# Kernel tuning notes

Hardware: AMD Instinct MI355X
Metric: run time of the kernel (lower is better)

## Reference

```python
import jax, jax.numpy as jnp
import numpy as np

EMB_DIM = 256
Q_DIM = 512
V_DIM = 512

def setup_inputs() -> dict:
    key = jax.random.key(0)
    ks = jax.random.split(key, 7)
    B, S = 8, 2048
    x = jax.random.normal(ks[0], (B, S, EMB_DIM), dtype=jnp.float32)
    s = 1.0 / np.sqrt(EMB_DIM)
    Wq = jax.random.normal(ks[1], (EMB_DIM, Q_DIM), dtype=jnp.float32) * s
    bq = jax.random.normal(ks[2], (Q_DIM,), dtype=jnp.float32) * 0.01
    Wk = jax.random.normal(ks[3], (EMB_DIM, Q_DIM), dtype=jnp.float32) * s
    bk = jax.random.normal(ks[4], (Q_DIM,), dtype=jnp.float32) * 0.01
    Wv = jax.random.normal(ks[5], (EMB_DIM, V_DIM), dtype=jnp.float32) * s
    bv = jax.random.normal(ks[6], (V_DIM,), dtype=jnp.float32) * 0.01
    return {"x": x, "Wq": Wq, "bq": bq, "Wk": Wk, "bk": bk, "Wv": Wv, "bv": bv}

def reference(x, Wq, bq, Wk, bk, Wv, bv):
    # q/k/v projections (torch Linear == x @ W + b with W stored [in, out] here)
    q = jax.nn.sigmoid(jnp.einsum('bse,eq->bsq', x, Wq) + bq)   # [B,S,Q]
    k = jnp.einsum('bse,eq->bsq', x, Wk) + bk                   # [B,S,Q]
    v = jnp.einsum('bse,ev->bsv', x, Wv) + bv                   # [B,S,V]
    scale = 1.0 / jnp.sqrt(jnp.float32(EMB_DIM))
    qk = jnp.einsum('bsq,btq->bst', q, k) * scale               # [B,S,S]
    qk = jax.nn.elu(qk)
    attn = jax.nn.softmax(qk, axis=-1)
    return jnp.einsum('bst,btv->bsv', attn, v)                  # [B,S,V]
```

## Files before the change

### kernel.cpp

```cpp
#include <hip/hip_runtime.h>
#include <hip/hip_bf16.h>
#include <math.h>

typedef unsigned short u16;
using short8 = __attribute__((ext_vector_type(8))) short;
using f32x4  = __attribute__((ext_vector_type(4))) float;

#define BM 128
#define BN 128
#define BK 32


__device__ __forceinline__ u16 f2bf(float f) {
  union { float f; unsigned u; } v; v.f = f;
  unsigned r = v.u + 0x7FFFu + ((v.u >> 16) & 1u);
  return (u16)(r >> 16);
}

__device__ __forceinline__ float fexp(float x) { return __expf(x); }

__device__ __forceinline__ void gld16(const void* g, void* l) {
  __builtin_amdgcn_global_load_lds(
      (const __attribute__((address_space(1))) void*)g,
      (__attribute__((address_space(3))) void*)l,
      16, 0, 0);
}


__device__ __forceinline__ void gemm_core(const u16* __restrict__ Ag,
                                          const u16* __restrict__ Bg,
                                          int K, u16* As, u16* Bs,
                                          f32x4 acc[4][4]) {
  const int tid = threadIdx.x;
  const int w = tid >> 6, l = tid & 63;
  const int wm = (w & 1) << 6, wn = (w >> 1) << 6;
  const int ln = l & 15, lq = l >> 4;
  const int sr0 = w * 16 + (l >> 2);
  const int sr1 = 64 + sr0;
  const int sk = (l & 3) * 8;

#pragma unroll
  for (int mt = 0; mt < 4; mt++)
#pragma unroll
    for (int nt = 0; nt < 4; nt++) acc[mt][nt] = (f32x4)0.0f;

  for (int k0 = 0; k0 < K; k0 += BK) {
    __syncthreads();
    gld16(Ag + (size_t)sr0 * K + k0 + sk, As + sr0 * BK + sk);
    gld16(Ag + (size_t)sr1 * K + k0 + sk, As + sr1 * BK + sk);
    gld16(Bg + (size_t)sr0 * K + k0 + sk, Bs + sr0 * BK + sk);
    gld16(Bg + (size_t)sr1 * K + k0 + sk, Bs + sr1 * BK + sk);
    __syncthreads();
    short8 af[4], bf[4];
#pragma unroll
    for (int mt = 0; mt < 4; mt++)
      af[mt] = *(const short8*)(As + (wm + mt * 16 + ln) * BK + lq * 8);
#pragma unroll
    for (int nt = 0; nt < 4; nt++)
      bf[nt] = *(const short8*)(Bs + (wn + nt * 16 + ln) * BK + lq * 8);
#pragma unroll
    for (int mt = 0; mt < 4; mt++)
#pragma unroll
      for (int nt = 0; nt < 4; nt++)
        acc[mt][nt] = __builtin_amdgcn_mfma_f32_16x16x32_bf16(
            af[mt], bf[nt], acc[mt][nt], 0, 0, 0);
  }
}


__global__ __launch_bounds__(256) void k_convx(const float* __restrict__ x,
                                               u16* __restrict__ xb, int n4) {
  int i = blockIdx.x * 256 + threadIdx.x;
  if (i < n4) {
    float4 v = ((const float4*)x)[i];
    ushort4 o;
    o.x = f2bf(v.x); o.y = f2bf(v.y); o.z = f2bf(v.z); o.w = f2bf(v.w);
    ((ushort4*)xb)[i] = o;
  }
}

__global__ __launch_bounds__(256) void k_convw(
    const float* __restrict__ Wq, const float* __restrict__ Wk,
    const float* __restrict__ Wv, const float* __restrict__ bq,
    const float* __restrict__ bk, const float* __restrict__ bv,
    u16* __restrict__ Wt, float* __restrict__ bcat) {
  int i = blockIdx.x * 256 + threadIdx.x;
  if (i < 1536 * 256) {
    int nn = i >> 8, e = i & 255;
    int sel = nn >> 9, c = nn & 511;
    const float* W = (sel == 0) ? Wq : (sel == 1) ? Wk : Wv;
    Wt[i] = f2bf(W[e * 512 + c]);
    if (e == 0) {
      const float* bb = (sel == 0) ? bq : (sel == 1) ? bk : bv;
      bcat[nn] = bb[c];
    }
  }
}


__global__ __launch_bounds__(256) void k_proj(
    const u16* __restrict__ xb, const u16* __restrict__ Wt,
    const float* __restrict__ bcat, u16* __restrict__ qb,
    u16* __restrict__ kb, u16* __restrict__ vb) {
  __shared__ __align__(16) u16 As[BM * BK];
  __shared__ __align__(16) u16 Bs[BN * BK];
  const int bm = blockIdx.y * BM, bn = blockIdx.x * BN;
  f32x4 acc[4][4];
  gemm_core(xb + (size_t)bm * 256, Wt + (size_t)bn * 256, 256, As, Bs, acc);

  const int tid = threadIdx.x, w = tid >> 6, l = tid & 63;
  const int wm = (w & 1) << 6, wn = (w >> 1) << 6;
  const int ln = l & 15, lq = l >> 4;
#pragma unroll
  for (int mt = 0; mt < 4; mt++)
#pragma unroll
    for (int r = 0; r < 4; r++) {
      int row = bm + wm + mt * 16 + lq * 4 + r;
#pragma unroll
      for (int nt = 0; nt < 4; nt++) {
        int col = bn + wn + nt * 16 + ln;
        float v = acc[mt][nt][r] + bcat[col];
        int sel = col >> 9, c2 = col & 511;
        float sg = __builtin_amdgcn_rcpf(1.0f + fexp(-v));
        float ov = (sel == 0) ? sg : v;
        u16* dst = (sel == 0) ? qb : (sel == 1) ? kb : vb;
        dst[(size_t)row * 512 + c2] = f2bf(ov);
      }
    }
}


__global__ __launch_bounds__(256) void k_transv(const u16* __restrict__ vb,
                                                u16* __restrict__ vtb) {
  const int b = blockIdx.z;
  const int t0 = blockIdx.y * 64, v0 = blockIdx.x * 64;
  __shared__ u16 tl[64][65];
  const u16* src = vb + (size_t)b * 2048 * 512;
  u16* dst = vtb + (size_t)b * 512 * 2048;
  for (int i = threadIdx.x; i < 4096; i += 256) {
    int r = i >> 6, c = i & 63;
    tl[r][c] = src[(size_t)(t0 + r) * 512 + v0 + c];
  }
  __syncthreads();
  for (int i = threadIdx.x; i < 4096; i += 256) {
    int r = i >> 6, c = i & 63;
    dst[(size_t)(v0 + r) * 2048 + t0 + c] = tl[c][r];
  }
}


__global__ __launch_bounds__(256) void k_qk(const u16* __restrict__ qb,
                                            const u16* __restrict__ kb,
                                            u16* __restrict__ P,
                                            float* __restrict__ lsum) {
  __shared__ __align__(16) u16 As[BM * BK];
  __shared__ __align__(16) u16 Bs[BN * BK];
  const int b = blockIdx.z;
  const int bm = blockIdx.y * BM, bn = blockIdx.x * BN;
  const size_t ob = (size_t)b * 2048 * 512;
  f32x4 acc[4][4];
  gemm_core(qb + ob + (size_t)bm * 512, kb + ob + (size_t)bn * 512, 512, As, Bs, acc);

  const int tid = threadIdx.x, w = tid >> 6, l = tid & 63;
  const int wm = (w & 1) << 6, wn = (w >> 1) << 6;
  const int ln = l & 15, lq = l >> 4;
  const float scale = 0.0625f;
#pragma unroll
  for (int mt = 0; mt < 4; mt++)
#pragma unroll
    for (int r = 0; r < 4; r++) {
      int row = bm + wm + mt * 16 + lq * 4 + r;
      float s = 0.0f;
#pragma unroll
      for (int nt = 0; nt < 4; nt++) {
        int col = bn + wn + nt * 16 + ln;
        float v = acc[mt][nt][r] * scale;
        float e = (v > 0.0f) ? v : (fexp(v) - 1.0f);
        float p = fexp(e);
        P[((size_t)b * 2048 + row) * 2048 + col] = f2bf(p);
        s += p;
      }
#pragma unroll
      for (int o = 1; o < 16; o <<= 1) s += __shfl_xor(s, o);
      if (ln == 0) atomicAdd(&lsum[b * 2048 + row], s);
    }
}


__global__ __launch_bounds__(256) void k_pv(const u16* __restrict__ P,
                                            const u16* __restrict__ vtb,
                                            const float* __restrict__ lsum,
                                            float* __restrict__ out) {
  __shared__ __align__(16) u16 As[BM * BK];
  __shared__ __align__(16) u16 Bs[BN * BK];
  const int b = blockIdx.z;
  const int bm = blockIdx.y * BM, bn = blockIdx.x * BN;
  f32x4 acc[4][4];
  gemm_core(P + (size_t)b * 2048 * 2048 + (size_t)bm * 2048,
            vtb + (size_t)b * 512 * 2048 + (size_t)bn * 2048, 2048, As, Bs, acc);

  const int tid = threadIdx.x, w = tid >> 6, l = tid & 63;
  const int wm = (w & 1) << 6, wn = (w >> 1) << 6;
  const int ln = l & 15, lq = l >> 4;
#pragma unroll
  for (int mt = 0; mt < 4; mt++)
#pragma unroll
    for (int r = 0; r < 4; r++) {
      int row = bm + wm + mt * 16 + lq * 4 + r;
      float inv = 1.0f / lsum[b * 2048 + row];
#pragma unroll
      for (int nt = 0; nt < 4; nt++) {
        int col = bn + wn + nt * 16 + ln;
        out[((size_t)b * 2048 + row) * 512 + col] = acc[mt][nt][r] * inv;
      }
    }
}


extern "C" void kernel_launch(void* const* d_in, const int* in_sizes, int n_in,
                              void* d_out, int out_size, void* d_ws, size_t ws_size,
                              hipStream_t stream) {
  const float* x  = (const float*)d_in[0];
  const float* Wq = (const float*)d_in[1];
  const float* bq = (const float*)d_in[2];
  const float* Wk = (const float*)d_in[3];
  const float* bk = (const float*)d_in[4];
  const float* Wv = (const float*)d_in[5];
  const float* bv = (const float*)d_in[6];
  float* out = (float*)d_out;
  char* ws = (char*)d_ws;

  u16*  qb   = (u16*)(ws + 0);
  u16*  kb   = (u16*)(ws + 16777216);
  u16*  vtb  = (u16*)(ws + 33554432);
  float* lsum = (float*)(ws + 50331648);
  u16*  P    = (u16*)(ws + 50397184);
  u16*  xb   = (u16*)(ws + 50397184);
  u16*  Wt   = (u16*)(ws + 58785792);
  float* bcat = (float*)(ws + 59572224);
  u16*  vb   = (u16*)(ws + 59578368);

  k_convx<<<4096, 256, 0, stream>>>(x, xb, 16384 * 256 / 4);
  k_convw<<<1536, 256, 0, stream>>>(Wq, Wk, Wv, bq, bk, bv, Wt, bcat);
  k_proj<<<dim3(12, 128, 1), 256, 0, stream>>>(xb, Wt, bcat, qb, kb, vb);
  k_transv<<<dim3(8, 32, 8), 256, 0, stream>>>(vb, vtb);
  hipMemsetAsync(lsum, 0, 16384 * sizeof(float), stream);
  k_qk<<<dim3(16, 16, 8), 256, 0, stream>>>(qb, kb, P, lsum);
  k_pv<<<dim3(4, 16, 8), 256, 0, stream>>>(P, vtb, lsum, out);
}
```

Measured before the change: 238.9 us.

## Split-K PV GEMM across two wave groups and vectorize V transpose

The PV kernel now runs 512 threads per block, with two 256-thread groups each covering half of the 2048-long K dimension; the partial accumulators are summed through shared memory before the normalized store. This doubles the wave count for the 512-block PV grid, which otherwise underfills the GPU, at the cost of an LDS reduction and extra syncs. The V transpose now moves four elements per access instead of one, and the projection epilogue hoists the q/k/v selection to block level.

After: 238.4 us. No clear change (-0.2%).

```diff
diff --git a/kernel.cpp b/kernel.cpp
--- a/kernel.cpp
+++ b/kernel.cpp
@@ -6,8 +6,6 @@
 using short8 = __attribute__((ext_vector_type(8))) short;
 using f32x4  = __attribute__((ext_vector_type(4))) float;
 
-#define BM 128
-#define BN 128
 #define BK 32
 
 
@@ -27,12 +25,11 @@
 }
 
 
-__device__ __forceinline__ void gemm_core(const u16* __restrict__ Ag,
-                                          const u16* __restrict__ Bg,
-                                          int K, u16* As, u16* Bs,
-                                          f32x4 acc[4][4]) {
-  const int tid = threadIdx.x;
-  const int w = tid >> 6, l = tid & 63;
+__device__ __forceinline__ void gemm_core4(const u16* __restrict__ Ag,
+                                           const u16* __restrict__ Bg,
+                                           int K, int lda, int ldb,
+                                           u16* As, u16* Bs,
+                                           f32x4 acc[4][4], int w, int l) {
   const int wm = (w & 1) << 6, wn = (w >> 1) << 6;
   const int ln = l & 15, lq = l >> 4;
   const int sr0 = w * 16 + (l >> 2);
@@ -46,10 +43,10 @@
 
   for (int k0 = 0; k0 < K; k0 += BK) {
     __syncthreads();
-    gld16(Ag + (size_t)sr0 * K + k0 + sk, As + sr0 * BK + sk);
-    gld16(Ag + (size_t)sr1 * K + k0 + sk, As + sr1 * BK + sk);
-    gld16(Bg + (size_t)sr0 * K + k0 + sk, Bs + sr0 * BK + sk);
-    gld16(Bg + (size_t)sr1 * K + k0 + sk, Bs + sr1 * BK + sk);
+    gld16(Ag + (size_t)sr0 * lda + k0 + sk, As + sr0 * BK + sk);
+    gld16(Ag + (size_t)sr1 * lda + k0 + sk, As + sr1 * BK + sk);
+    gld16(Bg + (size_t)sr0 * ldb + k0 + sk, Bs + sr0 * BK + sk);
+    gld16(Bg + (size_t)sr1 * ldb + k0 + sk, Bs + sr1 * BK + sk);
     __syncthreads();
     short8 af[4], bf[4];
 #pragma unroll
@@ -102,15 +99,19 @@
     const u16* __restrict__ xb, const u16* __restrict__ Wt,
     const float* __restrict__ bcat, u16* __restrict__ qb,
     u16* __restrict__ kb, u16* __restrict__ vb) {
-  __shared__ __align__(16) u16 As[BM * BK];
-  __shared__ __align__(16) u16 Bs[BN * BK];
-  const int bm = blockIdx.y * BM, bn = blockIdx.x * BN;
+  __shared__ __align__(16) u16 As[128 * BK];
+  __shared__ __align__(16) u16 Bs[128 * BK];
+  const int bm = blockIdx.y * 128, bn = blockIdx.x * 128;
+  const int tid = threadIdx.x, w = tid >> 6, l = tid & 63;
   f32x4 acc[4][4];
-  gemm_core(xb + (size_t)bm * 256, Wt + (size_t)bn * 256, 256, As, Bs, acc);
-
-  const int tid = threadIdx.x, w = tid >> 6, l = tid & 63;
+  gemm_core4(xb + (size_t)bm * 256, Wt + (size_t)bn * 256, 256, 256, 256,
+             As, Bs, acc, w, l);
+
   const int wm = (w & 1) << 6, wn = (w >> 1) << 6;
   const int ln = l & 15, lq = l >> 4;
+  const int sel = blockIdx.x >> 2;
+  u16* dst = (sel == 0) ? qb : (sel == 1) ? kb : vb;
+  const int cb = (blockIdx.x & 3) * 128;
 #pragma unroll
   for (int mt = 0; mt < 4; mt++)
 #pragma unroll
@@ -118,13 +119,10 @@
       int row = bm + wm + mt * 16 + lq * 4 + r;
 #pragma unroll
       for (int nt = 0; nt < 4; nt++) {
-        int col = bn + wn + nt * 16 + ln;
-        float v = acc[mt][nt][r] + bcat[col];
-        int sel = col >> 9, c2 = col & 511;
-        float sg = __builtin_amdgcn_rcpf(1.0f + fexp(-v));
-        float ov = (sel == 0) ? sg : v;
-        u16* dst = (sel == 0) ? qb : (sel == 1) ? kb : vb;
-        dst[(size_t)row * 512 + c2] = f2bf(ov);
+        int col = wn + nt * 16 + ln;
+        float v = acc[mt][nt][r] + bcat[bn + col];
+        float ov = (sel == 0) ? __builtin_amdgcn_rcpf(1.0f + fexp(-v)) : v;
+        dst[(size_t)row * 512 + cb + col] = f2bf(ov);
       }
     }
 }
@@ -134,17 +132,21 @@
                                                 u16* __restrict__ vtb) {
   const int b = blockIdx.z;
   const int t0 = blockIdx.y * 64, v0 = blockIdx.x * 64;
-  __shared__ u16 tl[64][65];
+  __shared__ u16 tl[64][68];
   const u16* src = vb + (size_t)b * 2048 * 512;
   u16* dst = vtb + (size_t)b * 512 * 2048;
-  for (int i = threadIdx.x; i < 4096; i += 256) {
-    int r = i >> 6, c = i & 63;
-    tl[r][c] = src[(size_t)(t0 + r) * 512 + v0 + c];
+  for (int i = threadIdx.x; i < 1024; i += 256) {
+    int r = i >> 4, c4 = (i & 15) * 4;
+    *(ushort4*)&tl[r][c4] =
+        *(const ushort4*)&src[(size_t)(t0 + r) * 512 + v0 + c4];
   }
   __syncthreads();
-  for (int i = threadIdx.x; i < 4096; i += 256) {
-    int r = i >> 6, c = i & 63;
-    dst[(size_t)(v0 + r) * 2048 + t0 + c] = tl[c][r];
+  for (int i = threadIdx.x; i < 1024; i += 256) {
+    int r = i >> 4, c4 = (i & 15) * 4;
+    ushort4 o;
+    o.x = tl[c4 + 0][r]; o.y = tl[c4 + 1][r];
+    o.z = tl[c4 + 2][r]; o.w = tl[c4 + 3][r];
+    *(ushort4*)&dst[(size_t)(v0 + r) * 2048 + t0 + c4] = o;
   }
 }
 
@@ -153,15 +155,16 @@
                                             const u16* __restrict__ kb,
                                             u16* __restrict__ P,
                                             float* __restrict__ lsum) {
-  __shared__ __align__(16) u16 As[BM * BK];
-  __shared__ __align__(16) u16 Bs[BN * BK];
+  __shared__ __align__(16) u16 As[128 * BK];
+  __shared__ __align__(16) u16 Bs[128 * BK];
   const int b = blockIdx.z;
-  const int bm = blockIdx.y * BM, bn = blockIdx.x * BN;
+  const int bm = blockIdx.y * 128, bn = blockIdx.x * 128;
   const size_t ob = (size_t)b * 2048 * 512;
+  const int tid = threadIdx.x, w = tid >> 6, l = tid & 63;
   f32x4 acc[4][4];
-  gemm_core(qb + ob + (size_t)bm * 512, kb + ob + (size_t)bn * 512, 512, As, Bs, acc);
-
-  const int tid = threadIdx.x, w = tid >> 6, l = tid & 63;
+  gemm_core4(qb + ob + (size_t)bm * 512, kb + ob + (size_t)bn * 512,
+             512, 512, 512, As, Bs, acc, w, l);
+
   const int wm = (w & 1) << 6, wn = (w >> 1) << 6;
   const int ln = l & 15, lq = l >> 4;
   const float scale = 0.0625f;
@@ -187,33 +190,62 @@
 }
 
 
-__global__ __launch_bounds__(256) void k_pv(const u16* __restrict__ P,
-                                            const u16* __restrict__ vtb,
-                                            const float* __restrict__ lsum,
-                                            float* __restrict__ out) {
-  __shared__ __align__(16) u16 As[BM * BK];
-  __shared__ __align__(16) u16 Bs[BN * BK];
+__global__ __launch_bounds__(512, 4) void k_pv(const u16* __restrict__ P,
+                                               const u16* __restrict__ vtb,
+                                               const float* __restrict__ lsum,
+                                               float* __restrict__ out) {
+  __shared__ __align__(16) u16 smem[16384];
   const int b = blockIdx.z;
-  const int bm = blockIdx.y * BM, bn = blockIdx.x * BN;
+  const int bm = blockIdx.y * 128, bn = blockIdx.x * 128;
+  const int tid = threadIdx.x;
+  const int g = tid >> 8;
+  const int t = tid & 255;
+  const int w = t >> 6, l = t & 63;
+  u16* As = smem + g * 8192;
+  u16* Bs = smem + g * 8192 + 4096;
+
   f32x4 acc[4][4];
-  gemm_core(P + (size_t)b * 2048 * 2048 + (size_t)bm * 2048,
-            vtb + (size_t)b * 512 * 2048 + (size_t)bn * 2048, 2048, As, Bs, acc);
-
-  const int tid = threadIdx.x, w = tid >> 6, l = tid & 63;
-  const int wm = (w & 1) << 6, wn = (w >> 1) << 6;
-  const int ln = l & 15, lq = l >> 4;
-#pragma unroll
-  for (int mt = 0; mt < 4; mt++)
-#pragma unroll
-    for (int r = 0; r < 4; r++) {
-      int row = bm + wm + mt * 16 + lq * 4 + r;
-      float inv = 1.0f / lsum[b * 2048 + row];
-#pragma unroll
-      for (int nt = 0; nt < 4; nt++) {
-        int col = bn + wn + nt * 16 + ln;
-        out[((size_t)b * 2048 + row) * 512 + col] = acc[mt][nt][r] * inv;
+  gemm_core4(P  + (size_t)b * 2048 * 2048 + (size_t)bm * 2048 + g * 1024,
+             vtb + (size_t)b * 512 * 2048 + (size_t)bn * 2048 + g * 1024,
+             1024, 2048, 2048, As, Bs, acc, w, l);
+
+  f32x4* red = (f32x4*)smem;
+#pragma unroll
+  for (int half = 0; half < 2; half++) {
+    __syncthreads();
+    if (g == 1) {
+#pragma unroll
+      for (int m2 = 0; m2 < 2; m2++)
+#pragma unroll
+        for (int nt = 0; nt < 4; nt++)
+          red[((m2 * 4 + nt) * 4 + w) * 64 + l] = acc[half * 2 + m2][nt];
+    }
+    __syncthreads();
+    if (g == 0) {
+#pragma unroll
+      for (int m2 = 0; m2 < 2; m2++)
+#pragma unroll
+        for (int nt = 0; nt < 4; nt++)
+          acc[half * 2 + m2][nt] += red[((m2 * 4 + nt) * 4 + w) * 64 + l];
+    }
+  }
+
+  if (g == 0) {
+    const int wm = (w & 1) << 6, wn = (w >> 1) << 6;
+    const int ln = l & 15, lq = l >> 4;
+#pragma unroll
+    for (int mt = 0; mt < 4; mt++)
+#pragma unroll
+      for (int r = 0; r < 4; r++) {
+        int row = bm + wm + mt * 16 + lq * 4 + r;
+        float inv = 1.0f / lsum[b * 2048 + row];
+#pragma unroll
+        for (int nt = 0; nt < 4; nt++) {
+          int col = bn + wn + nt * 16 + ln;
+          out[((size_t)b * 2048 + row) * 512 + col] = acc[mt][nt][r] * inv;
+        }
       }
-    }
+  }
 }
 
 
@@ -246,5 +278,5 @@
   k_transv<<<dim3(8, 32, 8), 256, 0, stream>>>(vb, vtb);
   hipMemsetAsync(lsum, 0, 16384 * sizeof(float), stream);
   k_qk<<<dim3(16, 16, 8), 256, 0, stream>>>(qb, kb, P, lsum);
-  k_pv<<<dim3(4, 16, 8), 256, 0, stream>>>(P, vtb, lsum, out);
-}
+  k_pv<<<dim3(4, 16, 8), 512, 0, stream>>>(P, vtb, lsum, out);
+}
```
